# Kernel tuning notes

Measured on AMD Instinct MI355X. Metric: run time of the kernel, lower is better.

## Reference

```python
import jax, jax.numpy as jnp
import numpy as np

H, N, SEQ = 256, 64, 4096

def setup_inputs() -> dict:
    key = jax.random.key(0)
    kA, kB, kC, kdt = jax.random.split(key, 4)
    W = jax.random.normal(kA, (H, N, N), dtype=jnp.float32)
    # Hurwitz (stable) A: skew-symmetric part minus 0.5*I, like HiPPO-style stable transitions
    A = 0.5 * (W - jnp.swapaxes(W, -1, -2)) - 0.5 * jnp.eye(N, dtype=jnp.float32)
    B = jax.random.normal(kB, (H, N), dtype=jnp.float32)
    C = jax.random.normal(kC, (H, N), dtype=jnp.float32)
    # log_dt around log(0.01), matching typical S4 timescale init
    log_dt = jax.random.normal(kdt, (H,), dtype=jnp.float32) * 0.5 + jnp.log(0.01)
    return {"A": A, "B": B, "C": C, "log_dt": log_dt, "L": SEQ}

def _bilinear(dt, A, B):
    # dt: (H,), A: (H,N,N), B: (H,N)
    n = A.shape[-1]
    I = jnp.eye(n, dtype=A.dtype)
    A_back = I - (dt[:, None, None] / 2) * A   # (H,N,N)
    A_fwd = I + (dt[:, None, None] / 2) * A    # (H,N,N)
    dA = jnp.linalg.solve(A_back, A_fwd)                       # (H,N,N)
    dB = dt[:, None] * jnp.linalg.solve(A_back, B[..., None])[..., 0]  # (H,N)
    return dA, dB

def _krylov(L, dA, dB, C):
    # K[h, l] = C[h] @ dA[h]^l @ dB[h], computed by squaring/doubling
    x = dB[..., None]  # (H, N, 1)
    A_ = dA
    while x.shape[-1] < L:
        x2 = jnp.einsum('hmn,hnl->hml', A_, x)  # apply current power
        x = jnp.concatenate([x, x2], axis=-1)
        if x.shape[-1] < L:
            A_ = jnp.einsum('hmn,hnk->hmk', A_, A_)  # square the power
    x = x[..., :L]  # (H, N, L)
    return jnp.einsum('hn,hnl->hl', C, x)  # (H, L)

def reference(A, B, C, log_dt, L):
    dt = jnp.exp(log_dt)
    dA, dB = _bilinear(dt, A, B)
    return _krylov(L, dA, dB, C)
```

## Files before the change

### kernel.cpp

```cpp
#include <hip/hip_runtime.h>

constexpr int STRU = 68;

typedef short v8s __attribute__((ext_vector_type(8)));
typedef float v4f __attribute__((ext_vector_type(4)));

__device__ __forceinline__ unsigned packhl(float x) {
    unsigned xb = __builtin_bit_cast(unsigned, x);
    unsigned t  = xb + 0x7fffu + ((xb >> 16) & 1u);
    unsigned hi = t & 0xffff0000u;
    float lof = x - __builtin_bit_cast(float, hi);
    unsigned lb = __builtin_bit_cast(unsigned, lof);
    unsigned lo = (lb + 0x7fffu + ((lb >> 16) & 1u)) >> 16;
    return hi | lo;
}

__device__ __forceinline__ float unpackf(unsigned v) {
    float h = __builtin_bit_cast(float, v & 0xffff0000u);
    float l = __builtin_bit_cast(float, v << 16);
    return h + l;
}

__device__ __forceinline__ void load_frag(const unsigned* p, v8s& hi, v8s& lo) {
    uint4 a = *(const uint4*)p;
    uint4 b = *(const uint4*)(p + 4);
    uint4 hw, lw;
    hw.x = __builtin_amdgcn_perm(a.y, a.x, 0x07060302u);
    hw.y = __builtin_amdgcn_perm(a.w, a.z, 0x07060302u);
    hw.z = __builtin_amdgcn_perm(b.y, b.x, 0x07060302u);
    hw.w = __builtin_amdgcn_perm(b.w, b.z, 0x07060302u);
    lw.x = __builtin_amdgcn_perm(a.y, a.x, 0x05040100u);
    lw.y = __builtin_amdgcn_perm(a.w, a.z, 0x05040100u);
    lw.z = __builtin_amdgcn_perm(b.y, b.x, 0x05040100u);
    lw.w = __builtin_amdgcn_perm(b.w, b.z, 0x05040100u);
    hi = __builtin_bit_cast(v8s, hw);
    lo = __builtin_bit_cast(v8s, lw);
}

#define MFMA __builtin_amdgcn_mfma_f32_16x16x32_bf16

template<int MODE>
__device__ __forceinline__ void mm64(const unsigned* P, const unsigned* Q,
                                     unsigned* D, float* G, int tid) {
    const int lane = tid & 63, w = tid >> 6;
    const int nh = lane & 15, qh = lane >> 4;
    const int tr0 = (w >> 1) << 1, tc0 = (w & 1) << 1;
    v4f acc[2][2] = {};
    #pragma unroll
    for (int kk = 0; kk < 2; ++kk) {
        const int kc = kk * 32 + qh * 8;
        v8s ph[2], pl[2], qhf[2], qlf[2];
        #pragma unroll
        for (int r = 0; r < 2; ++r)
            load_frag(P + ((tr0 + r) * 16 + nh) * STRU + kc, ph[r], pl[r]);
        #pragma unroll
        for (int c = 0; c < 2; ++c)
            load_frag(Q + ((tc0 + c) * 16 + nh) * STRU + kc, qhf[c], qlf[c]);
        #pragma unroll
        for (int r = 0; r < 2; ++r)
            #pragma unroll
            for (int c = 0; c < 2; ++c) {
                acc[r][c] = MFMA(ph[r], qhf[c], acc[r][c], 0, 0, 0);
                acc[r][c] = MFMA(ph[r], qlf[c], acc[r][c], 0, 0, 0);
                acc[r][c] = MFMA(pl[r], qhf[c], acc[r][c], 0, 0, 0);
            }
    }
    #pragma unroll
    for (int r = 0; r < 2; ++r)
        #pragma unroll
        for (int c = 0; c < 2; ++c) {
            const int col = (tc0 + c) * 16 + nh;
            #pragma unroll
            for (int e = 0; e < 4; ++e) {
                const int row = (tr0 + r) * 16 + qh * 4 + e;
                float v = acc[r][c][e];
                if constexpr (MODE == 1) { if (row == col) v += 1.0f; }
                if constexpr (MODE == 2) G[row * 64 + col] = v;
                else                     D[row * STRU + col] = packhl(v);
            }
        }
}

__device__ __forceinline__ void dbl64(unsigned* Xt, const unsigned* M, int k, int tid) {
    const int lane = tid & 63, w = tid >> 6;
    const int nh = lane & 15, qh = lane >> 4;
    const int tiles = (k + 15) >> 4;
    for (int t = 0; t < tiles; ++t) {
        v4f acc = {};
        #pragma unroll
        for (int kk = 0; kk < 2; ++kk) {
            const int kc = kk * 32 + qh * 8;
            v8s ph, pl, qhf, qlf;
            load_frag(Xt + (t * 16 + nh) * STRU + kc, ph, pl);
            load_frag(M + (w * 16 + nh) * STRU + kc, qhf, qlf);
            acc = MFMA(ph, qhf, acc, 0, 0, 0);
            acc = MFMA(ph, qlf, acc, 0, 0, 0);
            acc = MFMA(pl, qhf, acc, 0, 0, 0);
        }
        #pragma unroll
        for (int e = 0; e < 4; ++e) {
            const int j = t * 16 + qh * 4 + e;
            if (j < k) Xt[(k + j) * STRU + w * 16 + nh] = packhl(acc[e]);
        }
    }
}

__launch_bounds__(256)
__global__ void krylov_kernel(const float* __restrict__ A,
                              const float* __restrict__ Bv,
                              const float* __restrict__ Cv,
                              const float* __restrict__ logdt,
                              float* __restrict__ out)
{
    const int h    = blockIdx.x;
    const int tid  = threadIdx.x;
    const int lane = tid & 63;
    const int w    = tid >> 6;

    __shared__ __align__(16) unsigned SM[6][64 * STRU];
    __shared__ float Bl[64], Cl[64], t1s[64], t2s[64];

    const float dt = expf(logdt[h]);
    const float c  = 0.5f * dt;
    const float al = 1.0f + 0.5f * c;
    const float sd = -(c * c) / (al * al);
    const float c1 = 2.0f / al;
    const float c2 = 2.0f * c / (al * al);
    const float k1 = dt / al;
    const float k2 = dt * c / (al * al);

    const float* Ah = A + (size_t)h * 4096;

    for (int idx = tid; idx < 4096; idx += 256) {
        const int r = idx >> 6, cc = idx & 63;
        float v = Ah[idx] + (r == cc ? 0.5f : 0.0f);
        SM[0][r * STRU + cc] = packhl(v);
    }
    if (tid < 64) Bl[tid] = Bv[h * 64 + tid];
    else if (tid < 128) Cl[tid - 64] = Cv[h * 64 + tid - 64];
    __syncthreads();

    mm64<0>(SM[0], SM[0], SM[1], nullptr, tid);
    __syncthreads();

    for (int idx = tid; idx < 4096; idx += 256) {
        const int r = idx >> 6, cc = idx & 63;
        const int ad = r * STRU + cc;
        float dv = sd * unpackf(SM[1][ad]);
        SM[1][ad] = packhl(dv);
        SM[2][ad] = packhl(dv + (r == cc ? 1.0f : 0.0f));
    }
    __syncthreads();

    mm64<1>(SM[1], SM[2], SM[3], nullptr, tid);  __syncthreads();
    mm64<1>(SM[1], SM[3], SM[2], nullptr, tid);  __syncthreads();
    mm64<1>(SM[1], SM[2], SM[3], nullptr, tid);  __syncthreads();
    mm64<0>(SM[0], SM[3], SM[1], nullptr, tid);  __syncthreads();

    if (w == 0) {
        const unsigned* Tr = SM[3] + lane * STRU;
        float acc = 0.0f;
        #pragma unroll
        for (int m4 = 0; m4 < 16; ++m4) {
            uint4 tv = *(const uint4*)(Tr + 4 * m4);
            acc += unpackf(tv.x) * Bl[4 * m4 + 0] + unpackf(tv.y) * Bl[4 * m4 + 1]
                 + unpackf(tv.z) * Bl[4 * m4 + 2] + unpackf(tv.w) * Bl[4 * m4 + 3];
        }
        t1s[lane] = acc;
    } else if (w == 1) {
        const unsigned* Tr = SM[1] + lane * STRU;
        float acc = 0.0f;
        #pragma unroll
        for (int m4 = 0; m4 < 16; ++m4) {
            uint4 tv = *(const uint4*)(Tr + 4 * m4);
            acc += unpackf(tv.x) * Bl[4 * m4 + 0] + unpackf(tv.y) * Bl[4 * m4 + 1]
                 + unpackf(tv.z) * Bl[4 * m4 + 2] + unpackf(tv.w) * Bl[4 * m4 + 3];
        }
        t2s[lane] = acc;
    } else if (w == 2) {
        SM[5][lane] = packhl(Cl[lane]);
    }
    __syncthreads();

    for (int idx = tid; idx < 4096; idx += 256) {
        const int r = idx >> 6, cc = idx & 63;
        const int ad = r * STRU + cc;
        float tX = unpackf(SM[3][ad]);
        float sh = unpackf(SM[1][ad]);
        float dg = (r == cc) ? 1.0f : 0.0f;
        SM[0][ad] = packhl(c1 * tX + c2 * sh - dg);
        SM[2][ad] = packhl(c1 * tX - c2 * sh - dg);
    }
    if (tid < 64) SM[4][tid] = packhl(k1 * t1s[tid] + k2 * t2s[tid]);
    __syncthreads();

    int iX = 0, iXT = 2, iN = 1, iNT = 3;
    for (int s = 0; s < 6; ++s) {
        mm64<0>(SM[iX],  SM[iXT], SM[iN],  nullptr, tid);
        mm64<0>(SM[iXT], SM[iX],  SM[iNT], nullptr, tid);
        dbl64(SM[4], SM[iX], 1 << s, tid);
        __syncthreads();
        int t0 = iX;  iX  = iN;  iN  = t0;
        t0 = iXT; iXT = iNT; iNT = t0;
    }

    for (int s = 0; s < 6; ++s) {
        dbl64(SM[5], SM[iXT], 1 << s, tid);
        if (s < 5) {
            mm64<0>(SM[iX],  SM[iXT], SM[iN],  nullptr, tid);
            mm64<0>(SM[iXT], SM[iX],  SM[iNT], nullptr, tid);
        }
        __syncthreads();
        if (s < 5) {
            int t0 = iX;  iX  = iN;  iN  = t0;
            t0 = iXT; iXT = iNT; iNT = t0;
        }
    }

    mm64<2>(SM[5], SM[4], nullptr, out + (size_t)h * 4096, tid);
}

extern "C" void kernel_launch(void* const* d_in, const int* in_sizes, int n_in,
                              void* d_out, int out_size, void* d_ws, size_t ws_size,
                              hipStream_t stream) {
    const float* A  = (const float*)d_in[0];
    const float* B  = (const float*)d_in[1];
    const float* C  = (const float*)d_in[2];
    const float* ld = (const float*)d_in[3];
    float* out = (float*)d_out;
    const int H = in_sizes[3];
    krylov_kernel<<<H, 256, 0, stream>>>(A, B, C, ld, out);
}
```

Baseline: 93.48 us.

## Double block to 512 threads, fuse elementwise passes into matmul epilogues, compute transpose in-register

```diff
diff --git a/kernel.cpp b/kernel.cpp
--- a/kernel.cpp
+++ b/kernel.cpp
@@ -7,12 +7,10 @@
 
 __device__ __forceinline__ unsigned packhl(float x) {
     unsigned xb = __builtin_bit_cast(unsigned, x);
-    unsigned t  = xb + 0x7fffu + ((xb >> 16) & 1u);
-    unsigned hi = t & 0xffff0000u;
-    float lof = x - __builtin_bit_cast(float, hi);
-    unsigned lb = __builtin_bit_cast(unsigned, lof);
-    unsigned lo = (lb + 0x7fffu + ((lb >> 16) & 1u)) >> 16;
-    return hi | lo;
+    unsigned hb = xb & 0xffff0000u;
+    float lof = x - __builtin_bit_cast(float, hb);
+    unsigned lb = __builtin_bit_cast(unsigned, lof) + 0x8000u;
+    return __builtin_amdgcn_perm(xb, lb, 0x07060302u);
 }
 
 __device__ __forceinline__ float unpackf(unsigned v) {
@@ -40,72 +38,103 @@
 #define MFMA __builtin_amdgcn_mfma_f32_16x16x32_bf16
 
 template<int MODE>
-__device__ __forceinline__ void mm64(const unsigned* P, const unsigned* Q,
-                                     unsigned* D, float* G, int tid) {
+__device__ __forceinline__ void mm64(const unsigned* __restrict__ P,
+                                     const unsigned* __restrict__ Q,
+                                     unsigned* D, unsigned* DT, float* G,
+                                     const unsigned* R, float ca, float cb,
+                                     int tid) {
     const int lane = tid & 63, w = tid >> 6;
     const int nh = lane & 15, qh = lane >> 4;
-    const int tr0 = (w >> 1) << 1, tc0 = (w & 1) << 1;
-    v4f acc[2][2] = {};
+    const int tr = w >> 1, tc0 = (w & 1) << 1;
+    v4f acc[2] = {v4f{0,0,0,0}, v4f{0,0,0,0}};
     #pragma unroll
     for (int kk = 0; kk < 2; ++kk) {
         const int kc = kk * 32 + qh * 8;
-        v8s ph[2], pl[2], qhf[2], qlf[2];
-        #pragma unroll
-        for (int r = 0; r < 2; ++r)
-            load_frag(P + ((tr0 + r) * 16 + nh) * STRU + kc, ph[r], pl[r]);
-        #pragma unroll
-        for (int c = 0; c < 2; ++c)
-            load_frag(Q + ((tc0 + c) * 16 + nh) * STRU + kc, qhf[c], qlf[c]);
-        #pragma unroll
-        for (int r = 0; r < 2; ++r)
-            #pragma unroll
-            for (int c = 0; c < 2; ++c) {
-                acc[r][c] = MFMA(ph[r], qhf[c], acc[r][c], 0, 0, 0);
-                acc[r][c] = MFMA(ph[r], qlf[c], acc[r][c], 0, 0, 0);
-                acc[r][c] = MFMA(pl[r], qhf[c], acc[r][c], 0, 0, 0);
-            }
-    }
+        v8s ph, pl, q0h, q0l, q1h, q1l;
+        load_frag(P + (tr * 16 + nh) * STRU + kc, ph, pl);
+        load_frag(Q + (tc0 * 16 + nh) * STRU + kc, q0h, q0l);
+        load_frag(Q + ((tc0 + 1) * 16 + nh) * STRU + kc, q1h, q1l);
+        acc[0] = MFMA(ph, q0h, acc[0], 0, 0, 0);
+        acc[0] = MFMA(ph, q0l, acc[0], 0, 0, 0);
+        acc[0] = MFMA(pl, q0h, acc[0], 0, 0, 0);
+        acc[1] = MFMA(ph, q1h, acc[1], 0, 0, 0);
+        acc[1] = MFMA(ph, q1l, acc[1], 0, 0, 0);
+        acc[1] = MFMA(pl, q1h, acc[1], 0, 0, 0);
+    }
+    const int row0 = tr * 16 + qh * 4;
     #pragma unroll
-    for (int r = 0; r < 2; ++r)
-        #pragma unroll
-        for (int c = 0; c < 2; ++c) {
-            const int col = (tc0 + c) * 16 + nh;
-            #pragma unroll
-            for (int e = 0; e < 4; ++e) {
-                const int row = (tr0 + r) * 16 + qh * 4 + e;
-                float v = acc[r][c][e];
-                if constexpr (MODE == 1) { if (row == col) v += 1.0f; }
-                if constexpr (MODE == 2) G[row * 64 + col] = v;
-                else                     D[row * STRU + col] = packhl(v);
-            }
-        }
+    for (int c = 0; c < 2; ++c) {
+        const int col = (tc0 + c) * 16 + nh;
+        if constexpr (MODE == 2) {
+            #pragma unroll
+            for (int e = 0; e < 4; ++e) G[(row0 + e) * 64 + col] = acc[c][e];
+        } else if constexpr (MODE == 0) {
+            #pragma unroll
+            for (int e = 0; e < 4; ++e)
+                D[(row0 + e) * STRU + col] = packhl(acc[c][e]);
+        } else if constexpr (MODE == 1) {
+            #pragma unroll
+            for (int e = 0; e < 4; ++e) {
+                float v = acc[c][e] + ((row0 + e) == col ? 1.0f : 0.0f);
+                D[(row0 + e) * STRU + col] = packhl(v);
+            }
+        } else if constexpr (MODE == 3) {
+            uint4 tp;
+            #pragma unroll
+            for (int e = 0; e < 4; ++e) {
+                unsigned pk = packhl(acc[c][e]);
+                D[(row0 + e) * STRU + col] = pk;
+                ((unsigned*)&tp)[e] = pk;
+            }
+            *(uint4*)&DT[col * STRU + row0] = tp;
+        } else if constexpr (MODE == 4) {
+            #pragma unroll
+            for (int e = 0; e < 4; ++e) {
+                float dv = ca * acc[c][e];
+                float dg = ((row0 + e) == col) ? 1.0f : 0.0f;
+                D[(row0 + e) * STRU + col]  = packhl(dv);
+                DT[(row0 + e) * STRU + col] = packhl(dv + dg);
+            }
+        } else if constexpr (MODE == 5) {
+            #pragma unroll
+            for (int e = 0; e < 4; ++e) {
+                float t  = unpackf(R[(row0 + e) * STRU + col]);
+                float dg = ((row0 + e) == col) ? 1.0f : 0.0f;
+                float base = ca * t - dg;
+                float sv   = cb * acc[c][e];
+                D[(row0 + e) * STRU + col]  = packhl(base + sv);
+                DT[(row0 + e) * STRU + col] = packhl(base - sv);
+            }
+        }
+    }
 }
 
 __device__ __forceinline__ void dbl64(unsigned* Xt, const unsigned* M, int k, int tid) {
     const int lane = tid & 63, w = tid >> 6;
     const int nh = lane & 15, qh = lane >> 4;
-    const int tiles = (k + 15) >> 4;
-    for (int t = 0; t < tiles; ++t) {
-        v4f acc = {};
+    const int nt = (k + 15) >> 4;
+    if (w < 4 * nt) {
+        const int t = w >> 2, cb = w & 3;
+        v4f acc = {0, 0, 0, 0};
         #pragma unroll
         for (int kk = 0; kk < 2; ++kk) {
             const int kc = kk * 32 + qh * 8;
-            v8s ph, pl, qhf, qlf;
+            v8s ph, pl, mh, ml;
             load_frag(Xt + (t * 16 + nh) * STRU + kc, ph, pl);
-            load_frag(M + (w * 16 + nh) * STRU + kc, qhf, qlf);
-            acc = MFMA(ph, qhf, acc, 0, 0, 0);
-            acc = MFMA(ph, qlf, acc, 0, 0, 0);
-            acc = MFMA(pl, qhf, acc, 0, 0, 0);
+            load_frag(M + (cb * 16 + nh) * STRU + kc, mh, ml);
+            acc = MFMA(ph, mh, acc, 0, 0, 0);
+            acc = MFMA(ph, ml, acc, 0, 0, 0);
+            acc = MFMA(pl, mh, acc, 0, 0, 0);
         }
         #pragma unroll
         for (int e = 0; e < 4; ++e) {
             const int j = t * 16 + qh * 4 + e;
-            if (j < k) Xt[(k + j) * STRU + w * 16 + nh] = packhl(acc[e]);
-        }
-    }
-}
-
-__launch_bounds__(256)
+            if (j < k) Xt[(k + j) * STRU + cb * 16 + nh] = packhl(acc[e]);
+        }
+    }
+}
+
+__launch_bounds__(512)
 __global__ void krylov_kernel(const float* __restrict__ A,
                               const float* __restrict__ Bv,
                               const float* __restrict__ Cv,
@@ -118,7 +147,7 @@
     const int w    = tid >> 6;
 
     __shared__ __align__(16) unsigned SM[6][64 * STRU];
-    __shared__ float Bl[64], Cl[64], t1s[64], t2s[64];
+    __shared__ float Bl[64];
 
     const float dt = expf(logdt[h]);
     const float c  = 0.5f * dt;
@@ -126,98 +155,71 @@
     const float sd = -(c * c) / (al * al);
     const float c1 = 2.0f / al;
     const float c2 = 2.0f * c / (al * al);
-    const float k1 = dt / al;
-    const float k2 = dt * c / (al * al);
 
     const float* Ah = A + (size_t)h * 4096;
 
-    for (int idx = tid; idx < 4096; idx += 256) {
-        const int r = idx >> 6, cc = idx & 63;
-        float v = Ah[idx] + (r == cc ? 0.5f : 0.0f);
-        SM[0][r * STRU + cc] = packhl(v);
+    for (int idx = tid; idx < 1024; idx += 512) {
+        const int r = idx >> 4, c0 = (idx & 15) * 4;
+        float4 v = *(const float4*)(Ah + idx * 4);
+        if (r == c0 + 0) v.x += 0.5f;
+        if (r == c0 + 1) v.y += 0.5f;
+        if (r == c0 + 2) v.z += 0.5f;
+        if (r == c0 + 3) v.w += 0.5f;
+        uint4 pk = make_uint4(packhl(v.x), packhl(v.y), packhl(v.z), packhl(v.w));
+        *(uint4*)&SM[0][r * STRU + c0] = pk;
     }
     if (tid < 64) Bl[tid] = Bv[h * 64 + tid];
-    else if (tid < 128) Cl[tid - 64] = Cv[h * 64 + tid - 64];
-    __syncthreads();
-
-    mm64<0>(SM[0], SM[0], SM[1], nullptr, tid);
-    __syncthreads();
-
-    for (int idx = tid; idx < 4096; idx += 256) {
-        const int r = idx >> 6, cc = idx & 63;
-        const int ad = r * STRU + cc;
-        float dv = sd * unpackf(SM[1][ad]);
-        SM[1][ad] = packhl(dv);
-        SM[2][ad] = packhl(dv + (r == cc ? 1.0f : 0.0f));
-    }
-    __syncthreads();
-
-    mm64<1>(SM[1], SM[2], SM[3], nullptr, tid);  __syncthreads();
-    mm64<1>(SM[1], SM[3], SM[2], nullptr, tid);  __syncthreads();
-    mm64<1>(SM[1], SM[2], SM[3], nullptr, tid);  __syncthreads();
-    mm64<0>(SM[0], SM[3], SM[1], nullptr, tid);  __syncthreads();
+    else if (tid < 128) SM[5][tid - 64] = packhl(Cv[h * 64 + (tid - 64)]);
+    __syncthreads();
+
+    mm64<4>(SM[0], SM[0], SM[1], SM[2], nullptr, nullptr, sd, 0.f, tid);
+    __syncthreads();
+    mm64<1>(SM[1], SM[2], SM[3], nullptr, nullptr, nullptr, 0.f, 0.f, tid);
+    __syncthreads();
+    mm64<1>(SM[1], SM[3], SM[2], nullptr, nullptr, nullptr, 0.f, 0.f, tid);
+    __syncthreads();
+    mm64<1>(SM[1], SM[2], SM[3], nullptr, nullptr, nullptr, 0.f, 0.f, tid);
+    __syncthreads();
+    mm64<5>(SM[0], SM[3], SM[2], SM[1], nullptr, SM[3], c1, c2, tid);
+    __syncthreads();
 
     if (w == 0) {
-        const unsigned* Tr = SM[3] + lane * STRU;
+        const unsigned* Xr = SM[2] + lane * STRU;
         float acc = 0.0f;
         #pragma unroll
         for (int m4 = 0; m4 < 16; ++m4) {
-            uint4 tv = *(const uint4*)(Tr + 4 * m4);
-            acc += unpackf(tv.x) * Bl[4 * m4 + 0] + unpackf(tv.y) * Bl[4 * m4 + 1]
-                 + unpackf(tv.z) * Bl[4 * m4 + 2] + unpackf(tv.w) * Bl[4 * m4 + 3];
-        }
-        t1s[lane] = acc;
-    } else if (w == 1) {
-        const unsigned* Tr = SM[1] + lane * STRU;
-        float acc = 0.0f;
-        #pragma unroll
-        for (int m4 = 0; m4 < 16; ++m4) {
-            uint4 tv = *(const uint4*)(Tr + 4 * m4);
-            acc += unpackf(tv.x) * Bl[4 * m4 + 0] + unpackf(tv.y) * Bl[4 * m4 + 1]
-                 + unpackf(tv.z) * Bl[4 * m4 + 2] + unpackf(tv.w) * Bl[4 * m4 + 3];
-        }
-        t2s[lane] = acc;
-    } else if (w == 2) {
-        SM[5][lane] = packhl(Cl[lane]);
-    }
-    __syncthreads();
-
-    for (int idx = tid; idx < 4096; idx += 256) {
-        const int r = idx >> 6, cc = idx & 63;
-        const int ad = r * STRU + cc;
-        float tX = unpackf(SM[3][ad]);
-        float sh = unpackf(SM[1][ad]);
-        float dg = (r == cc) ? 1.0f : 0.0f;
-        SM[0][ad] = packhl(c1 * tX + c2 * sh - dg);
-        SM[2][ad] = packhl(c1 * tX - c2 * sh - dg);
-    }
-    if (tid < 64) SM[4][tid] = packhl(k1 * t1s[tid] + k2 * t2s[tid]);
-    __syncthreads();
-
-    int iX = 0, iXT = 2, iN = 1, iNT = 3;
+            uint4 xv = *(const uint4*)(Xr + 4 * m4);
+            float4 b4 = *(const float4*)&Bl[4 * m4];
+            acc += unpackf(xv.x) * b4.x + unpackf(xv.y) * b4.y
+                 + unpackf(xv.z) * b4.z + unpackf(xv.w) * b4.w;
+        }
+        SM[4][lane] = packhl(c * (acc + Bl[lane]));
+    }
+    __syncthreads();
+
+    unsigned *bX = SM[2], *bXT = SM[1], *bN = SM[0], *bNT = SM[3];
+    #pragma unroll 1
     for (int s = 0; s < 6; ++s) {
-        mm64<0>(SM[iX],  SM[iXT], SM[iN],  nullptr, tid);
-        mm64<0>(SM[iXT], SM[iX],  SM[iNT], nullptr, tid);
-        dbl64(SM[4], SM[iX], 1 << s, tid);
+        mm64<3>(bX, bXT, bN, bNT, nullptr, nullptr, 0.f, 0.f, tid);
+        dbl64(SM[4], bX, 1 << s, tid);
         __syncthreads();
-        int t0 = iX;  iX  = iN;  iN  = t0;
-        t0 = iXT; iXT = iNT; iNT = t0;
-    }
-
+        unsigned* t0 = bX;  bX  = bN;  bN  = t0;
+        t0 = bXT; bXT = bNT; bNT = t0;
+    }
+
+    #pragma unroll 1
     for (int s = 0; s < 6; ++s) {
-        dbl64(SM[5], SM[iXT], 1 << s, tid);
-        if (s < 5) {
-            mm64<0>(SM[iX],  SM[iXT], SM[iN],  nullptr, tid);
-            mm64<0>(SM[iXT], SM[iX],  SM[iNT], nullptr, tid);
-        }
+        if (s < 5) mm64<3>(bX, bXT, bN, bNT, nullptr, nullptr, 0.f, 0.f, tid);
+        dbl64(SM[5], bXT, 1 << s, tid);
         __syncthreads();
         if (s < 5) {
-            int t0 = iX;  iX  = iN;  iN  = t0;
-            t0 = iXT; iXT = iNT; iNT = t0;
-        }
-    }
-
-    mm64<2>(SM[5], SM[4], nullptr, out + (size_t)h * 4096, tid);
+            unsigned* t0 = bX;  bX  = bN;  bN  = t0;
+            t0 = bXT; bXT = bNT; bNT = t0;
+        }
+    }
+
+    mm64<2>(SM[5], SM[4], nullptr, nullptr, out + (size_t)h * 4096, nullptr,
+            0.f, 0.f, tid);
 }
 
 extern "C" void kernel_launch(void* const* d_in, const int* in_sizes, int n_in,
@@ -229,5 +231,5 @@
     const float* ld = (const float*)d_in[3];
     float* out = (float*)d_out;
     const int H = in_sizes[3];
-    krylov_kernel<<<H, 256, 0, stream>>>(A, B, C, ld, out);
-}
+    krylov_kernel<<<H, 512, 0, stream>>>(A, B, C, ld, out);
+}
```

New measurement: 79.63 us. 1.17x faster.
